# Kernel tuning notes

Hardware: AMD Instinct MI355X
Metric: run time of the kernel (lower is better)

## Reference

```python
import jax, jax.numpy as jnp
import numpy as np
from jax import lax

# dims
B, T, D = 2, 1024, 512
H, K, V = 8, 64, 64      # head_k_dim = head_v_dim = 64
CONV = 4
# IVON / module hyperparams (from __init__ defaults)
LR, B1, B2, WD, LAM = 1e-3, 0.9, 0.999, 0.0, 1.0
EPS = 1e-5               # RMSNorm eps
SCALE = K ** -0.5


def _silu(x):
    return x * jax.nn.sigmoid(x)


def _short_conv(x, w):
    """Causal depthwise conv1d (kernel_size=CONV, no bias) + SiLU. x:[B,T,C], w:[C,CONV]."""
    xp = jnp.pad(x, ((0, 0), (CONV - 1, 0), (0, 0)))
    y = sum(xp[:, i:i + x.shape[1]] * w[:, i] for i in range(CONV))
    return _silu(y)


def _l2norm(x):
    return x * lax.rsqrt(jnp.sum(x * x, -1, keepdims=True) + 1e-6)


def setup_inputs() -> dict:
    key = jax.random.key(0)
    ks = jax.random.split(key, 10)
    s = 0.02
    return {
        "hidden_states": jax.random.normal(ks[0], (B, T, D), jnp.float32),
        "Wq": jax.random.normal(ks[1], (D, H * K), jnp.float32) * s,
        "Wk": jax.random.normal(ks[2], (D, H * K), jnp.float32) * s,
        "Wv": jax.random.normal(ks[3], (D, H * V), jnp.float32) * s,
        "Wb": jax.random.normal(ks[4], (D, H), jnp.float32) * s,
        "cw_q": jax.random.normal(ks[5], (H * K, CONV), jnp.float32) * 0.5,
        "cw_k": jax.random.normal(ks[6], (H * K, CONV), jnp.float32) * 0.5,
        "cw_v": jax.random.normal(ks[7], (H * V, CONV), jnp.float32) * 0.5,
        "rms_w": jnp.ones((V,), jnp.float32),
        "Wo": jax.random.normal(ks[8], (H * V, D), jnp.float32) * s,
    }


def reference(hidden_states, Wq, Wk, Wv, Wb, cw_q, cw_k, cw_v, rms_w, Wo):
    x = hidden_states
    # projections -> causal depthwise short conv (+SiLU, qk_activation='silu')
    q = _short_conv(x @ Wq, cw_q).reshape(B, T, H, K)
    k = _short_conv(x @ Wk, cw_k).reshape(B, T, H, K)
    v = _short_conv(x @ Wv, cw_v).reshape(B, T, H, V)
    beta = jax.nn.sigmoid(x @ Wb)                     # [B,T,H]
    # qk l2-norm inside kernel (qk_norm='l2'), scale on q
    q = _l2norm(q) * SCALE
    k = _l2norm(k)

    # fused recurrent IVON delta-rule: per-step outer-product gradient of
    # 0.5||k @ S - v||^2, momentum g, diag preconditioner h (noise-free IVON).
    def step(carry, inp):
        S, h, g = carry                               # each [B,H,K,V]
        qt, kt, vt, bt = inp                          # [B,H,K],[B,H,K],[B,H,V],[B,H]
        pred = jnp.einsum('bhk,bhkv->bhv', kt, S)
        grad = kt[..., None] * (pred - vt)[..., None, :]   # [B,H,K,V]
        g = B1 * g + (1.0 - B1) * grad
        h = B2 * h + (1.0 - B2) * grad * grad
        S = S - LR * bt[..., None, None] * (g + WD * S) / (h + LAM)
        o = jnp.einsum('bhk,bhkv->bhv', qt, S)
        return (S, h, g), o

    z = jnp.zeros((B, H, K, V), jnp.float32)
    inps = (jnp.swapaxes(q, 0, 1), jnp.swapaxes(k, 0, 1),
            jnp.swapaxes(v, 0, 1), jnp.swapaxes(beta, 0, 1))
    _, o = lax.scan(step, (z, z, z), inps)            # o: [T,B,H,V]
    o = jnp.swapaxes(o, 0, 1)                          # [B,T,H,V]

    # RMSNorm over head_v_dim, then output projection
    o = o * lax.rsqrt(jnp.mean(o * o, -1, keepdims=True) + EPS) * rms_w
    o = o.reshape(B, T, H * V) @ Wo                    # [B,T,D]
    return o
```

## Files before the change

kernel.cpp:

```cpp
#include <hip/hip_runtime.h>
#include <hip/hip_bf16.h>
#include <math.h>

#define Bb 2
#define Tt 1024
#define Dd 512
#define Hh 8
#define Kk 64
#define Vv 64
#define BT (Bb*Tt)
#define HK (Hh*Kk)

#define B1c 0.9f
#define B2c 0.999f
#define LRc 1e-3f
#define SCALEc 0.125f

typedef short s8v __attribute__((ext_vector_type(8)));
typedef float f4v __attribute__((ext_vector_type(4)));

__device__ __forceinline__ unsigned short f2bf(float x) {
  unsigned u = __float_as_uint(x);
  u += 0x7FFFu + ((u >> 16) & 1u);
  return (unsigned short)(u >> 16);
}
__device__ __forceinline__ float bf2f(unsigned short h) {
  return __uint_as_float((unsigned)h << 16);
}

template <int CTRL>
__device__ __forceinline__ float dpp_add(float v) {
  int y = __builtin_amdgcn_update_dpp(0, __float_as_int(v), CTRL, 0xF, 0xF, true);
  return v + __int_as_float(y);
}

typedef unsigned uint2_t __attribute__((ext_vector_type(2)));

__device__ __forceinline__ float xor16_add(float x) {
#if __has_builtin(__builtin_amdgcn_permlane16_swap)
  uint2_t r = __builtin_amdgcn_permlane16_swap(__float_as_uint(x), __float_as_uint(x),
                                               false, false);
  return __uint_as_float(r.x) + __uint_as_float(r.y);
#else
  int y = __builtin_amdgcn_ds_swizzle(__float_as_int(x), 0x401F);
  return x + __int_as_float(y);
#endif
}

__device__ __forceinline__ float xor32_add(float x) {
#if __has_builtin(__builtin_amdgcn_permlane32_swap)
  uint2_t r = __builtin_amdgcn_permlane32_swap(__float_as_uint(x), __float_as_uint(x),
                                               false, false);
  return __uint_as_float(r.x) + __uint_as_float(r.y);
#else
  return x + __shfl_xor(x, 32, 64);
#endif
}

__device__ __forceinline__ float reduce16(float x) {
  x = dpp_add<0xB1>(x);
  x = dpp_add<0x4E>(x);
  x = dpp_add<0x141>(x);
  x = dpp_add<0x140>(x);
  return x;
}

__device__ __forceinline__ float reduce64(float x) {
  x = reduce16(x);
  x = xor16_add(x);
  x = xor32_add(x);
  return x;
}

__global__ __launch_bounds__(256) void cvt_x_kernel(
    const float* __restrict__ x, unsigned short* __restrict__ hi,
    unsigned short* __restrict__ lo) {
  const int i = (blockIdx.x * 256 + threadIdx.x) * 8;
  float4 a = *(const float4*)(x + i);
  float4 b = *(const float4*)(x + i + 4);
  const float v[8] = {a.x, a.y, a.z, a.w, b.x, b.y, b.z, b.w};
  union { unsigned short u[8]; uint4 q; } ph, pl;
#pragma unroll
  for (int j = 0; j < 8; ++j) {
    unsigned short h = f2bf(v[j]);
    ph.u[j] = h;
    pl.u[j] = f2bf(v[j] - bf2f(h));
  }
  *(uint4*)(hi + i) = ph.q;
  *(uint4*)(lo + i) = pl.q;
}

__global__ __launch_bounds__(256) void cvt_w_kernel(
    const float* __restrict__ W0, const float* __restrict__ W1,
    const float* __restrict__ W2,
    unsigned short* __restrict__ hib, unsigned short* __restrict__ lob) {
  __shared__ float Ts[64][65];
  const int z = blockIdx.z;
  const float* W = (z == 0) ? W0 : (z == 1) ? W1 : W2;
  unsigned short* hi = hib + (size_t)z * 512 * 512;
  unsigned short* lo = lob + (size_t)z * 512 * 512;
  const int tk = blockIdx.x * 64;
  const int tn = blockIdx.y * 64;
  const int r  = threadIdx.x >> 2;
  const int cg = threadIdx.x & 3;
#pragma unroll
  for (int j = 0; j < 4; ++j) {
    float4 v = *(const float4*)(W + (size_t)(tk + r) * 512 + tn + cg * 16 + j * 4);
    Ts[r][cg * 16 + j * 4 + 0] = v.x;
    Ts[r][cg * 16 + j * 4 + 1] = v.y;
    Ts[r][cg * 16 + j * 4 + 2] = v.z;
    Ts[r][cg * 16 + j * 4 + 3] = v.w;
  }
  __syncthreads();
  union { unsigned short u[16]; uint4 q[2]; } ph, pl;
#pragma unroll
  for (int j = 0; j < 16; ++j) {
    float v = Ts[cg * 16 + j][r];
    unsigned short h = f2bf(v);
    ph.u[j] = h;
    pl.u[j] = f2bf(v - bf2f(h));
  }
  const size_t ob = (size_t)(tn + r) * 512 + tk + cg * 16;
  *(uint4*)(hi + ob) = ph.q[0];
  *(uint4*)(hi + ob + 8) = ph.q[1];
  *(uint4*)(lo + ob) = pl.q[0];
  *(uint4*)(lo + ob + 8) = pl.q[1];
}

__device__ __forceinline__ void gemm_mfma_body(
    const unsigned short* __restrict__ Ahi, const unsigned short* __restrict__ Alo,
    const unsigned short* __restrict__ Bhi, const unsigned short* __restrict__ Blo,
    float* __restrict__ C) {
  __shared__ unsigned short Ah[64][40], Al[64][40], Bh[64][40], Bl[64][40];
  const int tid = threadIdx.x;
  const int bm = blockIdx.x * 64;
  const int bn = blockIdx.y * 64;
  const int srow = tid >> 2;
  const int skoff = (tid & 3) * 8;
  const int l = tid & 63, w = tid >> 6;
  const int arow = (l & 15) + 16 * w;
  const int koff = (l >> 4) * 8;

  const unsigned short* pAh = Ahi + (size_t)(bm + srow) * 512 + skoff;
  const unsigned short* pAl = Alo + (size_t)(bm + srow) * 512 + skoff;
  const unsigned short* pBh = Bhi + (size_t)(bn + srow) * 512 + skoff;
  const unsigned short* pBl = Blo + (size_t)(bn + srow) * 512 + skoff;

  f4v acc0 = {0.f, 0.f, 0.f, 0.f}, acc1 = acc0, acc2 = acc0, acc3 = acc0;

  uint4 rah = *(const uint4*)(pAh);
  uint4 ral = *(const uint4*)(pAl);
  uint4 rbh = *(const uint4*)(pBh);
  uint4 rbl = *(const uint4*)(pBl);

  for (int k0 = 0; k0 < 512; k0 += 32) {
    __syncthreads();
    *(uint4*)&Ah[srow][skoff] = rah;
    *(uint4*)&Al[srow][skoff] = ral;
    *(uint4*)&Bh[srow][skoff] = rbh;
    *(uint4*)&Bl[srow][skoff] = rbl;
    __syncthreads();
    if (k0 + 32 < 512) {
      rah = *(const uint4*)(pAh + k0 + 32);
      ral = *(const uint4*)(pAl + k0 + 32);
      rbh = *(const uint4*)(pBh + k0 + 32);
      rbl = *(const uint4*)(pBl + k0 + 32);
    }
    const s8v ah = *(const s8v*)&Ah[arow][koff];
    const s8v al = *(const s8v*)&Al[arow][koff];
#pragma unroll
    for (int c = 0; c < 4; ++c) {
      const s8v bh = *(const s8v*)&Bh[16 * c + (l & 15)][koff];
      const s8v bl = *(const s8v*)&Bl[16 * c + (l & 15)][koff];
      f4v* acc = (c == 0) ? &acc0 : (c == 1) ? &acc1 : (c == 2) ? &acc2 : &acc3;
      *acc = __builtin_amdgcn_mfma_f32_16x16x32_bf16(al, bh, *acc, 0, 0, 0);
      *acc = __builtin_amdgcn_mfma_f32_16x16x32_bf16(ah, bl, *acc, 0, 0, 0);
      *acc = __builtin_amdgcn_mfma_f32_16x16x32_bf16(ah, bh, *acc, 0, 0, 0);
    }
  }

  const int crow = bm + 16 * w + (l >> 4) * 4;
  const int ccol = bn + (l & 15);
#pragma unroll
  for (int i = 0; i < 4; ++i) {
    C[(size_t)(crow + i) * 512 + ccol + 0]  = acc0[i];
    C[(size_t)(crow + i) * 512 + ccol + 16] = acc1[i];
    C[(size_t)(crow + i) * 512 + ccol + 32] = acc2[i];
    C[(size_t)(crow + i) * 512 + ccol + 48] = acc3[i];
  }
}

__global__ __launch_bounds__(256) void gemm3_mfma_kernel(
    const unsigned short* __restrict__ xhi, const unsigned short* __restrict__ xlo,
    const unsigned short* __restrict__ whi, const unsigned short* __restrict__ wlo,
    float* __restrict__ qp, float* __restrict__ kp, float* __restrict__ vp) {
  const int z = blockIdx.z;
  float* Cp = (z == 0) ? qp : (z == 1) ? kp : vp;
  gemm_mfma_body(xhi, xlo, whi + (size_t)z * 512 * 512, wlo + (size_t)z * 512 * 512, Cp);
}

__global__ __launch_bounds__(256) void gemm1_mfma_kernel(
    const unsigned short* __restrict__ ahi, const unsigned short* __restrict__ alo,
    const unsigned short* __restrict__ whi, const unsigned short* __restrict__ wlo,
    float* __restrict__ C) {
  gemm_mfma_body(ahi, alo, whi, wlo, C);
}

__global__ __launch_bounds__(256) void beta_kernel(const float* __restrict__ x,
                                                   const float* __restrict__ Wb,
                                                   float* __restrict__ beta) {
  int gid = blockIdx.x * blockDim.x + threadIdx.x;
  int bt = gid >> 3, h = gid & 7;
  const float4* xr = (const float4*)(x + (size_t)bt * Dd);
  float s = 0.f;
#pragma unroll 4
  for (int d4 = 0; d4 < Dd / 4; ++d4) {
    float4 xv = xr[d4];
    const float* wb = Wb + (d4 * 4) * Hh + h;
    s = fmaf(xv.x, wb[0 * Hh], s);
    s = fmaf(xv.y, wb[1 * Hh], s);
    s = fmaf(xv.z, wb[2 * Hh], s);
    s = fmaf(xv.w, wb[3 * Hh], s);
  }
  beta[gid] = 1.f / (1.f + expf(-s));
}

__global__ __launch_bounds__(256) void conv_kernel(
    const float* __restrict__ qp, const float* __restrict__ kp,
    const float* __restrict__ vp,
    const float* __restrict__ cwq, const float* __restrict__ cwk,
    const float* __restrict__ cwv,
    float* __restrict__ qc, float* __restrict__ kc, float* __restrict__ vc) {
  const int mode = blockIdx.z;
  const float* pre; const float* cw; float* post;
  if (mode == 0)      { pre = qp; cw = cwq; post = qc; }
  else if (mode == 1) { pre = kp; cw = cwk; post = kc; }
  else                { pre = vp; cw = cwv; post = vc; }

  const int idx = blockIdx.x * 4 + (threadIdx.x >> 6);
  const int lane = threadIdx.x & 63;
  const int b = idx >> 13;
  const int th = idx & 8191;
  const int t = th >> 3;
  const int h = th & 7;
  const int ch = h * 64 + lane;

  float y = 0.f;
#pragma unroll
  for (int i = 0; i < 4; ++i) {
    int tt = t + i - 3;
    if (tt >= 0)
      y += pre[((size_t)(b * Tt + tt)) * HK + ch] * cw[ch * 4 + i];
  }
  y = y / (1.f + expf(-y));
  if (mode < 2) {
    float ss = reduce64(y * y);
    y *= rsqrtf(ss + 1e-6f);
    if (mode == 0) y *= SCALEc;
  }
  post[((size_t)(b * Tt + t)) * HK + ch] = y;
}

#define TC 16

__global__ __launch_bounds__(256) void scan_kernel(
    const float* __restrict__ qc, const float* __restrict__ kc,
    const float* __restrict__ vc, const float* __restrict__ beta,
    float* __restrict__ o) {
  __shared__ float4 ks[2][TC][16];
  __shared__ float4 qs[2][TC][16];
  __shared__ float2 vb[2][TC][16];

  const int tid  = threadIdx.x;
  const int lane = tid & 63;
  const int w    = tid >> 6;
  const int g    = lane & 15;
  const int cgrp = lane >> 4;
  const int bid  = blockIdx.x;
  const int vq   = bid >> 4;
  const int bh   = bid & 15;
  const int b = bh >> 3, h = bh & 7;
  const int colbase = vq * 16;
  const int cc = w * 4 + cgrp;
  const int v  = colbase + cc;

  const size_t base2 = ((size_t)b * Tt) * HK + h * 64;
  const float* bp = beta + ((size_t)b * Tt) * Hh + h;
  float* op = o + base2 + v;

  const int sr = tid >> 4;
  const int sg = tid & 15;

  {
    float4 k4 = *(const float4*)(kc + base2 + (size_t)sr * HK + sg * 4);
    float4 q4 = *(const float4*)(qc + base2 + (size_t)sr * HK + sg * 4);
    float  vv = vc[base2 + (size_t)sr * HK + colbase + sg];
    float  lb = (0.1f * LRc) * bp[(size_t)sr * Hh];
    ks[0][sr][sg] = k4;
    qs[0][sr][sg] = q4;
    vb[0][sr][sg] = make_float2(vv, lb);
    __syncthreads();
  }

  float S0 = 0, S1 = 0, S2 = 0, S3 = 0;
  float G0 = 0, G1 = 0, G2 = 0, G3 = 0;
  float H0 = 0, H1 = 0, H2 = 0, H3 = 0;
  float r0 = 1.f, r1 = 1.f, r2 = 1.f, r3 = 1.f;

  for (int tile = 0; tile < Tt / TC; ++tile) {
    const int d = tile & 1;
    const int t0 = tile * TC;
    const int more = (tile + 1 < Tt / TC);
    const int tn = more ? t0 + TC : t0;

    float4 nk = *(const float4*)(kc + base2 + (size_t)(tn + sr) * HK + sg * 4);
    float4 nq = *(const float4*)(qc + base2 + (size_t)(tn + sr) * HK + sg * 4);
    float  nv = vc[base2 + (size_t)(tn + sr) * HK + colbase + sg];
    float  nb = (0.1f * LRc) * bp[(size_t)(tn + sr) * Hh];

    float4 kt = ks[d][0][g];
    float pred = reduce16(fmaf(kt.x, S0,
                          fmaf(kt.y, S1,
                          fmaf(kt.z, S2, kt.w * S3))));

#pragma unroll
    for (int s = 0; s < TC; ++s) {
      const float4 kv = ks[d][s][g];
      const float4 qv = qs[d][s][g];
      const float2 vbc = vb[d][s][cc];
      const float vv = vbc.x, lrb = vbc.y;

      const float diff = pred - vv;
      const float gr0 = kv.x * diff;
      const float gr1 = kv.y * diff;
      const float gr2 = kv.z * diff;
      const float gr3 = kv.w * diff;
      G0 = fmaf(B1c, G0, gr0);
      G1 = fmaf(B1c, G1, gr1);
      G2 = fmaf(B1c, G2, gr2);
      G3 = fmaf(B1c, G3, gr3);
      H0 = fmaf(B2c, H0, gr0 * gr0);
      H1 = fmaf(B2c, H1, gr1 * gr1);
      H2 = fmaf(B2c, H2, gr2 * gr2);
      H3 = fmaf(B2c, H3, gr3 * gr3);
      const float d0 = fmaf(H0, 0.001f, 1.0f);
      const float d1 = fmaf(H1, 0.001f, 1.0f);
      const float d2 = fmaf(H2, 0.001f, 1.0f);
      const float d3 = fmaf(H3, 0.001f, 1.0f);
      r0 = r0 * fmaf(-d0, r0, 2.0f);
      r1 = r1 * fmaf(-d1, r1, 2.0f);
      r2 = r2 * fmaf(-d2, r2, 2.0f);
      r3 = r3 * fmaf(-d3, r3, 2.0f);
      S0 = fmaf(-lrb, G0 * r0, S0);
      S1 = fmaf(-lrb, G1 * r1, S1);
      S2 = fmaf(-lrb, G2 * r2, S2);
      S3 = fmaf(-lrb, G3 * r3, S3);

      float po = fmaf(qv.x, S0,
                 fmaf(qv.y, S1,
                 fmaf(qv.z, S2, qv.w * S3)));
      if (s + 1 < TC) {
        const float4 k1 = ks[d][s + 1][g];
        float pp = fmaf(k1.x, S0,
                   fmaf(k1.y, S1,
                   fmaf(k1.z, S2, k1.w * S3)));
        po = dpp_add<0xB1>(po);   pp = dpp_add<0xB1>(pp);
        po = dpp_add<0x4E>(po);   pp = dpp_add<0x4E>(pp);
        po = dpp_add<0x141>(po);  pp = dpp_add<0x141>(pp);
        po = dpp_add<0x140>(po);  pp = dpp_add<0x140>(pp);
        pred = pp;
      } else {
        po = reduce16(po);
      }
      op[(size_t)(t0 + s) * HK] = po;
    }

    if (more) {
      ks[d ^ 1][sr][sg] = nk;
      qs[d ^ 1][sr][sg] = nq;
      vb[d ^ 1][sr][sg] = make_float2(nv, nb);
    }
    __syncthreads();
  }
}

__global__ __launch_bounds__(256) void rmsnorm_kernel(
    const float* __restrict__ o, const float* __restrict__ rmsw,
    unsigned short* __restrict__ hi, unsigned short* __restrict__ lo) {
  const int idx = blockIdx.x * 4 + (threadIdx.x >> 6);
  const int lane = threadIdx.x & 63;
  const float* p = o + (size_t)idx * 64;
  float y = p[lane];
  float ss = reduce64(y * y);
  y = y * rsqrtf(ss * (1.f / 64.f) + 1e-5f) * rmsw[lane];
  unsigned short h = f2bf(y);
  hi[(size_t)idx * 64 + lane] = h;
  lo[(size_t)idx * 64 + lane] = f2bf(y - bf2f(h));
}

extern "C" void kernel_launch(void* const* d_in, const int* in_sizes, int n_in,
                              void* d_out, int out_size, void* d_ws, size_t ws_size,
                              hipStream_t stream) {
  const float* x    = (const float*)d_in[0];
  const float* Wq   = (const float*)d_in[1];
  const float* Wk   = (const float*)d_in[2];
  const float* Wv   = (const float*)d_in[3];
  const float* Wb   = (const float*)d_in[4];
  const float* cwq  = (const float*)d_in[5];
  const float* cwk  = (const float*)d_in[6];
  const float* cwv  = (const float*)d_in[7];
  const float* rmsw = (const float*)d_in[8];
  const float* Wo   = (const float*)d_in[9];
  float* out = (float*)d_out;
  float* ws  = (float*)d_ws;

  const size_t SZ = (size_t)BT * HK;
  float* qp   = ws;
  float* kp   = ws + 1 * SZ;
  float* vp   = ws + 2 * SZ;
  float* qc   = ws + 3 * SZ;
  float* kc   = ws + 4 * SZ;
  float* vc   = ws + 5 * SZ;
  float* beta = ws + 6 * SZ;
  float* on   = qp;

  unsigned short* xhi  = (unsigned short*)qc;
  unsigned short* xlo  = xhi + SZ;
  unsigned short* wh3  = (unsigned short*)kc;
  unsigned short* wl3  = wh3 + 3 * 512 * 512;
  unsigned short* wohi = (unsigned short*)vc;
  unsigned short* wolo = wohi + 512 * 512;
  unsigned short* onhi = (unsigned short*)kp;
  unsigned short* onlo = (unsigned short*)vp;

  cvt_x_kernel<<<dim3(BT * Dd / (256 * 8)), 256, 0, stream>>>(x, xhi, xlo);
  cvt_w_kernel<<<dim3(8, 8, 3), 256, 0, stream>>>(Wq, Wk, Wv, wh3, wl3);
  gemm3_mfma_kernel<<<dim3(BT / 64, HK / 64, 3), 256, 0, stream>>>(
      xhi, xlo, wh3, wl3, qp, kp, vp);
  beta_kernel<<<dim3(BT * Hh / 256), 256, 0, stream>>>(x, Wb, beta);
  conv_kernel<<<dim3(Bb * Tt * Hh / 4, 1, 3), 256, 0, stream>>>(
      qp, kp, vp, cwq, cwk, cwv, qc, kc, vc);
  scan_kernel<<<dim3(Bb * Hh * (Vv / 16)), 256, 0, stream>>>(
      qc, kc, vc, beta, on);
  cvt_w_kernel<<<dim3(8, 8, 1), 256, 0, stream>>>(Wo, Wo, Wo, wohi, wolo);
  rmsnorm_kernel<<<dim3(Bb * Tt * Hh / 4), 256, 0, stream>>>(on, rmsw, onhi, onlo);
  gemm1_mfma_kernel<<<dim3(BT / 64, HK / 64, 1), 256, 0, stream>>>(
      onhi, onlo, wohi, wolo, out);
}
```

Measured before the change: 214.9 us.

## Map one state element per lane in scan, quadrupling scan block count

```diff
diff --git a/kernel.cpp b/kernel.cpp
--- a/kernel.cpp
+++ b/kernel.cpp
@@ -267,22 +267,18 @@
     const float* __restrict__ qc, const float* __restrict__ kc,
     const float* __restrict__ vc, const float* __restrict__ beta,
     float* __restrict__ o) {
-  __shared__ float4 ks[2][TC][16];
-  __shared__ float4 qs[2][TC][16];
-  __shared__ float2 vb[2][TC][16];
+  __shared__ float ks[2][TC][64];
+  __shared__ float qs[2][TC][64];
+  __shared__ float2 vb[2][TC][4];
 
   const int tid  = threadIdx.x;
   const int lane = tid & 63;
   const int w    = tid >> 6;
-  const int g    = lane & 15;
-  const int cgrp = lane >> 4;
   const int bid  = blockIdx.x;
   const int vq   = bid >> 4;
   const int bh   = bid & 15;
   const int b = bh >> 3, h = bh & 7;
-  const int colbase = vq * 16;
-  const int cc = w * 4 + cgrp;
-  const int v  = colbase + cc;
+  const int v  = vq * 4 + w;
 
   const size_t base2 = ((size_t)b * Tt) * HK + h * 64;
   const float* bp = beta + ((size_t)b * Tt) * Hh + h;
@@ -290,22 +286,23 @@
 
   const int sr = tid >> 4;
   const int sg = tid & 15;
+  const int vr = tid >> 2;
+  const int vcc = tid & 3;
 
   {
     float4 k4 = *(const float4*)(kc + base2 + (size_t)sr * HK + sg * 4);
     float4 q4 = *(const float4*)(qc + base2 + (size_t)sr * HK + sg * 4);
-    float  vv = vc[base2 + (size_t)sr * HK + colbase + sg];
-    float  lb = (0.1f * LRc) * bp[(size_t)sr * Hh];
-    ks[0][sr][sg] = k4;
-    qs[0][sr][sg] = q4;
-    vb[0][sr][sg] = make_float2(vv, lb);
+    *(float4*)&ks[0][sr][sg * 4] = k4;
+    *(float4*)&qs[0][sr][sg * 4] = q4;
+    if (tid < 64) {
+      float vv = vc[base2 + (size_t)vr * HK + vq * 4 + vcc];
+      float lb = (0.1f * LRc) * bp[(size_t)vr * Hh];
+      vb[0][vr][vcc] = make_float2(vv, lb);
+    }
     __syncthreads();
   }
 
-  float S0 = 0, S1 = 0, S2 = 0, S3 = 0;
-  float G0 = 0, G1 = 0, G2 = 0, G3 = 0;
-  float H0 = 0, H1 = 0, H2 = 0, H3 = 0;
-  float r0 = 1.f, r1 = 1.f, r2 = 1.f, r3 = 1.f;
+  float S = 0.f, G = 0.f, H = 0.f, r = 1.f;
 
   for (int tile = 0; tile < Tt / TC; ++tile) {
     const int d = tile & 1;
@@ -315,70 +312,49 @@
 
     float4 nk = *(const float4*)(kc + base2 + (size_t)(tn + sr) * HK + sg * 4);
     float4 nq = *(const float4*)(qc + base2 + (size_t)(tn + sr) * HK + sg * 4);
-    float  nv = vc[base2 + (size_t)(tn + sr) * HK + colbase + sg];
-    float  nb = (0.1f * LRc) * bp[(size_t)(tn + sr) * Hh];
-
-    float4 kt = ks[d][0][g];
-    float pred = reduce16(fmaf(kt.x, S0,
-                          fmaf(kt.y, S1,
-                          fmaf(kt.z, S2, kt.w * S3))));
+    float nv = 0.f, nb = 0.f;
+    if (tid < 64) {
+      nv = vc[base2 + (size_t)(tn + vr) * HK + vq * 4 + vcc];
+      nb = (0.1f * LRc) * bp[(size_t)(tn + vr) * Hh];
+    }
+
+    float pred = reduce64(ks[d][0][lane] * S);
 
 #pragma unroll
     for (int s = 0; s < TC; ++s) {
-      const float4 kv = ks[d][s][g];
-      const float4 qv = qs[d][s][g];
-      const float2 vbc = vb[d][s][cc];
-      const float vv = vbc.x, lrb = vbc.y;
-
-      const float diff = pred - vv;
-      const float gr0 = kv.x * diff;
-      const float gr1 = kv.y * diff;
-      const float gr2 = kv.z * diff;
-      const float gr3 = kv.w * diff;
-      G0 = fmaf(B1c, G0, gr0);
-      G1 = fmaf(B1c, G1, gr1);
-      G2 = fmaf(B1c, G2, gr2);
-      G3 = fmaf(B1c, G3, gr3);
-      H0 = fmaf(B2c, H0, gr0 * gr0);
-      H1 = fmaf(B2c, H1, gr1 * gr1);
-      H2 = fmaf(B2c, H2, gr2 * gr2);
-      H3 = fmaf(B2c, H3, gr3 * gr3);
-      const float d0 = fmaf(H0, 0.001f, 1.0f);
-      const float d1 = fmaf(H1, 0.001f, 1.0f);
-      const float d2 = fmaf(H2, 0.001f, 1.0f);
-      const float d3 = fmaf(H3, 0.001f, 1.0f);
-      r0 = r0 * fmaf(-d0, r0, 2.0f);
-      r1 = r1 * fmaf(-d1, r1, 2.0f);
-      r2 = r2 * fmaf(-d2, r2, 2.0f);
-      r3 = r3 * fmaf(-d3, r3, 2.0f);
-      S0 = fmaf(-lrb, G0 * r0, S0);
-      S1 = fmaf(-lrb, G1 * r1, S1);
-      S2 = fmaf(-lrb, G2 * r2, S2);
-      S3 = fmaf(-lrb, G3 * r3, S3);
-
-      float po = fmaf(qv.x, S0,
-                 fmaf(qv.y, S1,
-                 fmaf(qv.z, S2, qv.w * S3)));
+      const float kv = ks[d][s][lane];
+      const float qv = qs[d][s][lane];
+      const float2 vbc = vb[d][s][w];
+
+      const float diff = pred - vbc.x;
+      const float lrb = vbc.y;
+      const float gr = kv * diff;
+      G = fmaf(B1c, G, gr);
+      H = fmaf(B2c, H, gr * gr);
+      const float dd = fmaf(H, 0.001f, 1.0f);
+      r = r * fmaf(-dd, r, 2.0f);
+      S = fmaf(-lrb, G * r, S);
+
+      float po = qv * S;
       if (s + 1 < TC) {
-        const float4 k1 = ks[d][s + 1][g];
-        float pp = fmaf(k1.x, S0,
-                   fmaf(k1.y, S1,
-                   fmaf(k1.z, S2, k1.w * S3)));
+        float pp = ks[d][s + 1][lane] * S;
         po = dpp_add<0xB1>(po);   pp = dpp_add<0xB1>(pp);
         po = dpp_add<0x4E>(po);   pp = dpp_add<0x4E>(pp);
         po = dpp_add<0x141>(po);  pp = dpp_add<0x141>(pp);
         po = dpp_add<0x140>(po);  pp = dpp_add<0x140>(pp);
+        po = xor16_add(po);       pp = xor16_add(pp);
+        po = xor32_add(po);       pp = xor32_add(pp);
         pred = pp;
       } else {
-        po = reduce16(po);
+        po = reduce64(po);
       }
       op[(size_t)(t0 + s) * HK] = po;
     }
 
     if (more) {
-      ks[d ^ 1][sr][sg] = nk;
-      qs[d ^ 1][sr][sg] = nq;
-      vb[d ^ 1][sr][sg] = make_float2(nv, nb);
+      *(float4*)&ks[d ^ 1][sr][sg * 4] = nk;
+      *(float4*)&qs[d ^ 1][sr][sg * 4] = nq;
+      if (tid < 64) vb[d ^ 1][vr][vcc] = make_float2(nv, nb);
     }
     __syncthreads();
   }
@@ -440,7 +416,7 @@
   beta_kernel<<<dim3(BT * Hh / 256), 256, 0, stream>>>(x, Wb, beta);
   conv_kernel<<<dim3(Bb * Tt * Hh / 4, 1, 3), 256, 0, stream>>>(
       qp, kp, vp, cwq, cwk, cwv, qc, kc, vc);
-  scan_kernel<<<dim3(Bb * Hh * (Vv / 16)), 256, 0, stream>>>(
+  scan_kernel<<<dim3(Bb * Hh * (Vv / 4)), 256, 0, stream>>>(
       qc, kc, vc, beta, on);
   cvt_w_kernel<<<dim3(8, 8, 1), 256, 0, stream>>>(Wo, Wo, Wo, wohi, wolo);
   rmsnorm_kernel<<<dim3(Bb * Tt * Hh / 4), 256, 0, stream>>>(on, rmsw, onhi, onlo);
```

New measurement: 208.1 us. 3.2% less time.
